# Kernel optimization log

Measured on AMD Instinct MI355X. Metric: run time of the kernel, lower is better.

The kernel has to match this reference:

```python
import jax, jax.numpy as jnp
import numpy as np

DT = 1.0       # integration timestep
THRESH = 0.5   # firing threshold (standard in this family of SNN repos)


def setup_inputs() -> dict:
    key = jax.random.key(0)
    ks = jax.random.split(key, 6)
    B, Din, Dout = 32768, 256, 512
    input_spike = jax.random.uniform(ks[0], (B, Din), dtype=jnp.float32)
    mem = jnp.zeros((B, Dout), jnp.float32)
    spike = jnp.zeros((B, Dout), jnp.float32)
    s_in = 1.0 / np.sqrt(Din)
    s_h = 1.0 / np.sqrt(Dout)
    W_dense = jax.random.uniform(ks[1], (Dout, Din), minval=-s_in, maxval=s_in, dtype=jnp.float32)
    b_dense = jax.random.uniform(ks[2], (Dout,), minval=-s_in, maxval=s_in, dtype=jnp.float32)
    W_rec = jax.random.uniform(ks[3], (Dout, Dout), minval=-s_h, maxval=s_h, dtype=jnp.float32)
    b_rec = jax.random.uniform(ks[4], (Dout,), minval=-s_h, maxval=s_h, dtype=jnp.float32)
    tau_m = 20.0 + 5.0 * jax.random.normal(ks[5], (Dout,), dtype=jnp.float32)
    return dict(input_spike=input_spike, mem=mem, spike=spike,
                W_dense=W_dense, b_dense=b_dense, W_rec=W_rec, b_rec=b_rec,
                tau_m=tau_m)


def reference(input_spike, mem, spike, W_dense, b_dense, W_rec, b_rec, tau_m):
    # d_input = dense(input_spike) + recurrent(spike)
    d_input = (jnp.einsum('bi,oi->bo', input_spike, W_dense) + b_dense
               + jnp.einsum('bh,oh->bo', spike, W_rec) + b_rec)
    # LIF neuron dynamics: exponential membrane decay, soft reset, heaviside spike
    alpha = jnp.exp(-DT / tau_m)                                   # [Dout]
    mem_new = mem * alpha + (1.0 - alpha) * d_input - THRESH * spike
    spike_new = (mem_new - THRESH > 0).astype(mem_new.dtype)
    return mem_new, spike_new
```

## Files before the change

### kernel.cpp

```cpp
#include <hip/hip_runtime.h>
#include <math.h>

typedef short  short8  __attribute__((ext_vector_type(8)));
typedef short  short4v __attribute__((ext_vector_type(4)));
typedef float  f32x4   __attribute__((ext_vector_type(4)));

#define BATCH 32768
#define DIN   256
#define DOUT  512
#define BM    128
#define BN    64

#define WS_FLAGS 0
#define WS_WD2   4096
#define WS_WR2   (4096 + 262144)
#define WS_X2    (266240 + 524288)

__device__ __forceinline__ short f2bf(float v) {
    unsigned u = __float_as_uint(v);
    u += 0x7fffu + ((u >> 16) & 1u);
    return (short)(u >> 16);
}

__device__ __forceinline__ void gload_lds16(const void* g, void* l) {
    __builtin_amdgcn_global_load_lds(
        (const __attribute__((address_space(1))) unsigned int*)g,
        (__attribute__((address_space(3))) unsigned int*)l, 16, 0, 0);
}

__global__ __launch_bounds__(256) void prepass_kernel(
    const float* __restrict__ SPK, const float* __restrict__ X,
    const float* __restrict__ Wd,  const float* __restrict__ Wr,
    int* __restrict__ flags, short* __restrict__ X2,
    short* __restrict__ Wd2, short* __restrict__ Wr2)
{
    const int b   = blockIdx.x;
    const int tid = threadIdx.x;

    {
        unsigned bits = 0;
        const f32x4* p = (const f32x4*)SPK + (size_t)b * 2048;
#pragma unroll
        for (int j = 0; j < 8; j++) {
            f32x4 v = p[tid + j * 256];
            bits |= __float_as_uint(v[0]) | __float_as_uint(v[1])
                  | __float_as_uint(v[2]) | __float_as_uint(v[3]);
        }
        if (__any(bits != 0) && (tid & 63) == 0)
            atomicOr(&flags[b >> 3], 1);
    }

    {
        const f32x4* src = (const f32x4*)X + (size_t)b * 1024;
        short4v*     dst = (short4v*)X2   + (size_t)b * 1024;
#pragma unroll
        for (int j = 0; j < 4; j++) {
            f32x4 v = src[tid + j * 256];
            dst[tid + j * 256] = (short4v){f2bf(v[0]), f2bf(v[1]),
                                           f2bf(v[2]), f2bf(v[3])};
        }
    }

    {
        int idx = b * 256 + tid;
        if (idx < 32768) {
            f32x4 v = ((const f32x4*)Wd)[idx];
            ((short4v*)Wd2)[idx] = (short4v){f2bf(v[0]), f2bf(v[1]),
                                             f2bf(v[2]), f2bf(v[3])};
        } else if (idx < 98304) {
            int k = idx - 32768;
            f32x4 v = ((const f32x4*)Wr)[k];
            ((short4v*)Wr2)[k] = (short4v){f2bf(v[0]), f2bf(v[1]),
                                           f2bf(v[2]), f2bf(v[3])};
        }
    }
}

__global__ __launch_bounds__(256, 3) void spike_rnn_lif_kernel(
    const short* __restrict__ X2,
    const float* __restrict__ MEM,
    const float* __restrict__ SPK,
    const short* __restrict__ Wd2,
    const float* __restrict__ bd,
    const short* __restrict__ Wr2,
    const float* __restrict__ br,
    const float* __restrict__ tau,
    const int*   __restrict__ flags,
    float* __restrict__ out)
{
    __shared__ __align__(16) char smem[49152];
    float* sT = (float*)smem;

    const int tid  = threadIdx.x;
    const int lane = tid & 63;
    const int w    = tid >> 6;
    const int wm   = w & 1;
    const int wn   = w >> 1;

    const int L    = blockIdx.x;
    const int bm   = ((L >> 6) << 3) + (L & 7);
    const int bn   = (L >> 3) & 7;
    const int m0   = bm * BM;
    const int n0   = bn * BN;
    const int col  = lane & 15;
    const int quad = lane >> 4;

    const bool has_spk = (flags[bm] != 0);

#define STAGE(c0, buf)                                                        \
    do {                                                                      \
        _Pragma("unroll")                                                     \
        for (int i = 0; i < 4; i++) {                                         \
            int seg = w * 4 + i;                                              \
            int r   = seg * 8 + (lane >> 3);                                  \
            const char* src = (const char*)X2 + (size_t)(m0 + r) * 512        \
                + (c0) * 128 + (((lane & 7) * 16) ^ ((r & 7) << 4));          \
            gload_lds16(src, (buf) + seg * 1024);                             \
        }                                                                     \
        _Pragma("unroll")                                                     \
        for (int i = 0; i < 2; i++) {                                         \
            int seg = w * 2 + i;                                              \
            int r   = seg * 8 + (lane >> 3);                                  \
            const char* src = (const char*)Wd2 + (size_t)(n0 + r) * 512       \
                + (c0) * 128 + (((lane & 7) * 16) ^ ((r & 7) << 4));          \
            gload_lds16(src, (buf) + 16384 + seg * 1024);                     \
        }                                                                     \
    } while (0)

    STAGE(0, smem);

    const int c4   = tid & 15;
    const int ncol = n0 + c4 * 4;
    f32x4 mv0[4], mv1[4];
#pragma unroll
    for (int it = 0; it < 4; it++) {
        int r2 = (tid + it * 256) >> 4;
        mv0[it] = __builtin_nontemporal_load(
                      (const f32x4*)(MEM + (size_t)(m0 + r2) * DOUT + ncol));
        mv1[it] = __builtin_nontemporal_load(
                      (const f32x4*)(MEM + (size_t)(m0 + 64 + r2) * DOUT + ncol));
    }

    f32x4 acc[4][2];
#pragma unroll
    for (int i = 0; i < 4; i++)
#pragma unroll
        for (int j = 0; j < 2; j++)
            acc[i][j] = (f32x4){0.f, 0.f, 0.f, 0.f};

    const int swz  = (col & 7) << 4;
    const int arow = wm * 64 + col;
    const int brow = wn * 32 + col;

#define DSLOAD(buf, kk, aa, bb)                                               \
    do {                                                                      \
        int ko = (quad * 16 + (kk) * 64) ^ swz;                               \
        _Pragma("unroll")                                                     \
        for (int t = 0; t < 4; t++)                                           \
            aa[t] = *(const short8*)((buf) + (arow + t * 16) * 128 + ko);     \
        _Pragma("unroll")                                                     \
        for (int t = 0; t < 2; t++)                                           \
            bb[t] = *(const short8*)((buf) + 16384 + (brow + t * 16) * 128 + ko); \
    } while (0)

#define MFMA_AB(aa, bb)                                                       \
    do {                                                                      \
        _Pragma("unroll")                                                     \
        for (int i = 0; i < 4; i++)                                           \
            _Pragma("unroll")                                                 \
            for (int j = 0; j < 2; j++)                                       \
                acc[i][j] = __builtin_amdgcn_mfma_f32_16x16x32_bf16(          \
                    aa[i], bb[j], acc[i][j], 0, 0, 0);                        \
    } while (0)

    short8 a0[4], b0[2], a1[4], b1[2];

    __syncthreads();
#pragma unroll
    for (int c = 0; c < 4; c++) {
        char* cur = smem + (c & 1) * 24576;
        if (c < 3) {
            char* nxt = smem + ((c + 1) & 1) * 24576;
            STAGE(c + 1, nxt);
        }
        DSLOAD(cur, 0, a0, b0);
        DSLOAD(cur, 1, a1, b1);
        MFMA_AB(a0, b0);
        MFMA_AB(a1, b1);
        if (c < 3) __syncthreads();
    }
#undef DSLOAD
#undef STAGE

    if (has_spk) {
        const float* Abase = SPK + (size_t)(m0 + wm * 64 + col) * DOUT + quad * 8;
        const short* Bbase = Wr2 + (size_t)(n0 + wn * 32 + col) * DOUT + quad * 8;
#pragma unroll 4
        for (int ks = 0; ks < 16; ks++) {
            int k = ks * 32;
            short8 a[4], b[2];
#pragma unroll
            for (int t = 0; t < 4; t++) {
                const float* ap = Abase + (size_t)t * 16 * DOUT + k;
                f32x4 lo = *(const f32x4*)ap;
                f32x4 hi = *(const f32x4*)(ap + 4);
                a[t] = (short8){f2bf(lo[0]), f2bf(lo[1]), f2bf(lo[2]), f2bf(lo[3]),
                                f2bf(hi[0]), f2bf(hi[1]), f2bf(hi[2]), f2bf(hi[3])};
            }
#pragma unroll
            for (int t = 0; t < 2; t++)
                b[t] = *(const short8*)(Bbase + (size_t)t * 16 * DOUT + k);
            MFMA_AB(a, b);
        }
    }
#undef MFMA_AB

    float al[4], oma[4], bs[4];
#pragma unroll
    for (int q = 0; q < 4; q++) {
        al[q]  = expf(-1.0f / tau[ncol + q]);
        oma[q] = 1.0f - al[q];
        bs[q]  = bd[ncol + q] + br[ncol + q];
    }

#pragma unroll
    for (int c = 0; c < 2; c++) {
        if (c) __syncthreads();
        if (wm == c) {
#pragma unroll
            for (int j = 0; j < 2; j++)
#pragma unroll
                for (int i = 0; i < 4; i++)
#pragma unroll
                    for (int rr = 0; rr < 4; rr++)
                        sT[(i * 16 + quad * 4 + rr) * 68 + wn * 32 + j * 16 + col]
                            = acc[i][j][rr];
        }
        __syncthreads();
#pragma unroll
        for (int it = 0; it < 4; it++) {
            int p   = tid + it * 256;
            int r2  = p >> 4;
            int row = m0 + c * 64 + r2;
            f32x4 d  = *(const f32x4*)(sT + r2 * 68 + c4 * 4);
            f32x4 mv = c ? mv1[it] : mv0[it];
            f32x4 sv = has_spk ? *(const f32x4*)(SPK + (size_t)row * DOUT + ncol)
                               : (f32x4){0.f, 0.f, 0.f, 0.f};
            f32x4 mn, sp;
#pragma unroll
            for (int q = 0; q < 4; q++) {
                mn[q] = mv[q] * al[q] + oma[q] * (d[q] + bs[q]) - 0.5f * sv[q];
                sp[q] = (mn[q] - 0.5f > 0.0f) ? 1.0f : 0.0f;
            }
            __builtin_nontemporal_store(mn,
                (f32x4*)(out + (size_t)row * DOUT + ncol));
            __builtin_nontemporal_store(sp,
                (f32x4*)(out + (size_t)BATCH * DOUT + (size_t)row * DOUT + ncol));
        }
    }
}

extern "C" void kernel_launch(void* const* d_in, const int* in_sizes, int n_in,
                              void* d_out, int out_size, void* d_ws, size_t ws_size,
                              hipStream_t stream) {
    const float* X   = (const float*)d_in[0];
    const float* MEM = (const float*)d_in[1];
    const float* SPK = (const float*)d_in[2];
    const float* Wd  = (const float*)d_in[3];
    const float* bd  = (const float*)d_in[4];
    const float* Wr  = (const float*)d_in[5];
    const float* br  = (const float*)d_in[6];
    const float* tau = (const float*)d_in[7];

    char*  ws    = (char*)d_ws;
    int*   flags = (int*)  (ws + WS_FLAGS);
    short* Wd2   = (short*)(ws + WS_WD2);
    short* Wr2   = (short*)(ws + WS_WR2);
    short* X2    = (short*)(ws + WS_X2);

    hipMemsetAsync(flags, 0, 256 * sizeof(int), stream);
    prepass_kernel<<<2048, 256, 0, stream>>>(SPK, X, Wd, Wr, flags, X2, Wd2, Wr2);

    spike_rnn_lif_kernel<<<2048, 256, 0, stream>>>(X2, MEM, SPK, Wd2, bd, Wr2, br,
                                                   tau, flags, (float*)d_out);
}
```

Measured before the change: 274.9 us.

## Drop LDS double buffering to single buffer and raise occupancy to 4 blocks

The dense-GEMM K loop goes from two 24 KB LDS stages to one, which halves shared memory to 24 KB per block and raises the launch bound from 3 to 4 blocks per CU. Each chunk now computes from the single buffer, then synchronises, issues the next global-to-LDS load and synchronises again, so loads no longer overlap the MFMAs within a block. The aim is to hide that latency with more resident blocks and fewer live registers (one A/B fragment set instead of two). An extra barrier is added before the epilogue reuses the shared buffer.

```diff
diff --git a/kernel.cpp b/kernel.cpp
--- a/kernel.cpp
+++ b/kernel.cpp
@@ -76,7 +76,7 @@
     }
 }
 
-__global__ __launch_bounds__(256, 3) void spike_rnn_lif_kernel(
+__global__ __launch_bounds__(256, 4) void spike_rnn_lif_kernel(
     const short* __restrict__ X2,
     const float* __restrict__ MEM,
     const float* __restrict__ SPK,
@@ -88,7 +88,7 @@
     const int*   __restrict__ flags,
     float* __restrict__ out)
 {
-    __shared__ __align__(16) char smem[49152];
+    __shared__ __align__(16) char smem[24576];
     float* sT = (float*)smem;
 
     const int tid  = threadIdx.x;
@@ -107,7 +107,7 @@
 
     const bool has_spk = (flags[bm] != 0);
 
-#define STAGE(c0, buf)                                                        \
+#define STAGE(c0)                                                             \
     do {                                                                      \
         _Pragma("unroll")                                                     \
         for (int i = 0; i < 4; i++) {                                         \
@@ -115,7 +115,7 @@
             int r   = seg * 8 + (lane >> 3);                                  \
             const char* src = (const char*)X2 + (size_t)(m0 + r) * 512        \
                 + (c0) * 128 + (((lane & 7) * 16) ^ ((r & 7) << 4));          \
-            gload_lds16(src, (buf) + seg * 1024);                             \
+            gload_lds16(src, smem + seg * 1024);                              \
         }                                                                     \
         _Pragma("unroll")                                                     \
         for (int i = 0; i < 2; i++) {                                         \
@@ -123,11 +123,11 @@
             int r   = seg * 8 + (lane >> 3);                                  \
             const char* src = (const char*)Wd2 + (size_t)(n0 + r) * 512       \
                 + (c0) * 128 + (((lane & 7) * 16) ^ ((r & 7) << 4));          \
-            gload_lds16(src, (buf) + 16384 + seg * 1024);                     \
+            gload_lds16(src, smem + 16384 + seg * 1024);                      \
         }                                                                     \
     } while (0)
 
-    STAGE(0, smem);
+    STAGE(0);
 
     const int c4   = tid & 15;
     const int ncol = n0 + c4 * 4;
@@ -152,15 +152,15 @@
     const int arow = wm * 64 + col;
     const int brow = wn * 32 + col;
 
-#define DSLOAD(buf, kk, aa, bb)                                               \
+#define DSLOAD(kk, aa, bb)                                                    \
     do {                                                                      \
         int ko = (quad * 16 + (kk) * 64) ^ swz;                               \
         _Pragma("unroll")                                                     \
         for (int t = 0; t < 4; t++)                                           \
-            aa[t] = *(const short8*)((buf) + (arow + t * 16) * 128 + ko);     \
+            aa[t] = *(const short8*)(smem + (arow + t * 16) * 128 + ko);      \
         _Pragma("unroll")                                                     \
         for (int t = 0; t < 2; t++)                                           \
-            bb[t] = *(const short8*)((buf) + 16384 + (brow + t * 16) * 128 + ko); \
+            bb[t] = *(const short8*)(smem + 16384 + (brow + t * 16) * 128 + ko); \
     } while (0)
 
 #define MFMA_AB(aa, bb)                                                       \
@@ -173,21 +173,20 @@
                     aa[i], bb[j], acc[i][j], 0, 0, 0);                        \
     } while (0)
 
-    short8 a0[4], b0[2], a1[4], b1[2];
+    short8 a0[4], b0[2];
 
     __syncthreads();
 #pragma unroll
     for (int c = 0; c < 4; c++) {
-        char* cur = smem + (c & 1) * 24576;
+        DSLOAD(0, a0, b0);
+        MFMA_AB(a0, b0);
+        DSLOAD(1, a0, b0);
+        MFMA_AB(a0, b0);
         if (c < 3) {
-            char* nxt = smem + ((c + 1) & 1) * 24576;
-            STAGE(c + 1, nxt);
-        }
-        DSLOAD(cur, 0, a0, b0);
-        DSLOAD(cur, 1, a1, b1);
-        MFMA_AB(a0, b0);
-        MFMA_AB(a1, b1);
-        if (c < 3) __syncthreads();
+            __syncthreads();
+            STAGE(c + 1);
+            __syncthreads();
+        }
     }
 #undef DSLOAD
 #undef STAGE
@@ -222,6 +221,8 @@
         oma[q] = 1.0f - al[q];
         bs[q]  = bd[ncol + q] + br[ncol + q];
     }
+
+    __syncthreads();
 
 #pragma unroll
     for (int c = 0; c < 2; c++) {
```

Result: slower. 281.8 us (+2.5%).
